# Kernel optimization log

Hardware: AMD Instinct MI355X
Metric: run time of the kernel (lower is better)

## Reference

```python
import jax, jax.numpy as jnp
import numpy as np

LR = 0.01        # memory update learning rate (init kwarg lr)
INIT_SCALE = 0.01
B, N, D = 8, 1024, 256


def setup_inputs() -> dict:
    key = jax.random.key(0)
    k1, k2, k3, k4, k5 = jax.random.split(key, 5)
    return {
        "sequence": jax.random.normal(k1, (B, N, D), dtype=jnp.float32),
        "targets": jax.random.normal(k2, (B, N, D), dtype=jnp.float32),
        "theta0": jax.random.normal(k3, (D, D), dtype=jnp.float32) * INIT_SCALE,
        "W_e": jax.random.normal(k4, (D, D), dtype=jnp.float32) * INIT_SCALE,
        "W_o": jax.random.normal(k5, (D, D), dtype=jnp.float32) * INIT_SCALE,
    }


def reference(sequence, targets, theta0, W_e, W_o):
    # process_sequence on (batch, n, d) with targets: theta is reset to theta0
    # for each batch element, then updated sequentially per token (delta rule).
    def step(theta, xt):
        x_t, tgt_t = xt                      # (d,), (d,)
        h = W_e @ x_t                        # encode: F.linear(x, W_e)
        pred = theta @ h                     # predict with current memory
        err = tgt_t - pred
        theta_new = theta + LR * jnp.outer(err, h)   # rank-1 fast-weight update
        out = W_o @ pred                     # output projection of PREDICTION
        return theta_new, out

    def per_batch(seq_b, tgt_b):             # (n, d), (n, d)
        _, outs = jax.lax.scan(step, theta0, (seq_b, tgt_b))
        return outs                          # (n, d)

    return jax.vmap(per_batch)(sequence, targets)   # (batch, n, d)
```

## Files before the change

### kernel.cpp

```cpp
#include <hip/hip_runtime.h>

#define LR_C 0.01f
#define NB 8
#define NTOK 1024
#define DD 256
#define CH 8
#define NCHUNK (NTOK / CH)

#define DPP_ADD(x, ctrl) \
    ((x) + __int_as_float(__builtin_amdgcn_update_dpp( \
        0, __float_as_int(x), (ctrl), 0xF, 0xF, true)))

#define REDUCE_ALL64(s) do { \
    s = DPP_ADD(s, 0xB1); \
    s = DPP_ADD(s, 0x4E); \
    s = DPP_ADD(s, 0x141); \
    s = DPP_ADD(s, 0x140); \
    s += __shfl_xor(s, 16, 64); \
    s += __shfl_xor(s, 32, 64); \
} while (0)

#define TBM 64
#define TBN 64
#define TBK 16

__global__ __launch_bounds__(256) void gemm_abt_kernel(
    const float* __restrict__ A, const float* __restrict__ B,
    float* __restrict__ C)
{
    __shared__ float As[TBK][TBM + 4];
    __shared__ float Bs[TBK][TBN + 4];
    const int t    = threadIdx.x;
    const int lrow = t >> 2, lk = (t & 3) * 4;
    const int tx   = t & 15, ty = t >> 4;

    const float* Ap = A + (size_t)(blockIdx.x * TBM + lrow) * DD + lk;
    const float* Bp = B + (size_t)(blockIdx.y * TBN + lrow) * DD + lk;

    float4 acc[4];
    #pragma unroll
    for (int i = 0; i < 4; ++i) acc[i] = make_float4(0.f, 0.f, 0.f, 0.f);

    float4 a0 = *reinterpret_cast<const float4*>(Ap);
    float4 b0 = *reinterpret_cast<const float4*>(Bp);

    for (int k0 = 0; k0 < DD; k0 += TBK) {
        __syncthreads();
        As[lk + 0][lrow] = a0.x; As[lk + 1][lrow] = a0.y;
        As[lk + 2][lrow] = a0.z; As[lk + 3][lrow] = a0.w;
        Bs[lk + 0][lrow] = b0.x; Bs[lk + 1][lrow] = b0.y;
        Bs[lk + 2][lrow] = b0.z; Bs[lk + 3][lrow] = b0.w;
        __syncthreads();
        if (k0 + TBK < DD) {
            a0 = *reinterpret_cast<const float4*>(Ap + k0 + TBK);
            b0 = *reinterpret_cast<const float4*>(Bp + k0 + TBK);
        }
        #pragma unroll
        for (int k = 0; k < TBK; ++k) {
            float4 av = *reinterpret_cast<const float4*>(&As[k][ty * 4]);
            float4 bv = *reinterpret_cast<const float4*>(&Bs[k][tx * 4]);
            acc[0].x = fmaf(av.x, bv.x, acc[0].x); acc[0].y = fmaf(av.x, bv.y, acc[0].y);
            acc[0].z = fmaf(av.x, bv.z, acc[0].z); acc[0].w = fmaf(av.x, bv.w, acc[0].w);
            acc[1].x = fmaf(av.y, bv.x, acc[1].x); acc[1].y = fmaf(av.y, bv.y, acc[1].y);
            acc[1].z = fmaf(av.y, bv.z, acc[1].z); acc[1].w = fmaf(av.y, bv.w, acc[1].w);
            acc[2].x = fmaf(av.z, bv.x, acc[2].x); acc[2].y = fmaf(av.z, bv.y, acc[2].y);
            acc[2].z = fmaf(av.z, bv.z, acc[2].z); acc[2].w = fmaf(av.z, bv.w, acc[2].w);
            acc[3].x = fmaf(av.w, bv.x, acc[3].x); acc[3].y = fmaf(av.w, bv.y, acc[3].y);
            acc[3].z = fmaf(av.w, bv.z, acc[3].z); acc[3].w = fmaf(av.w, bv.w, acc[3].w);
        }
    }
    #pragma unroll
    for (int i = 0; i < 4; ++i) {
        float* cp = C + (size_t)(blockIdx.x * TBM + ty * 4 + i) * DD
                      + blockIdx.y * TBN + tx * 4;
        *reinterpret_cast<float4*>(cp) = acc[i];
    }
}

__global__ __launch_bounds__(256) void gemm_pt_kernel(
    const float* __restrict__ PT, const float* __restrict__ B,
    float* __restrict__ C)
{
    __shared__ float As[TBK][TBM + 4];
    __shared__ float Bs[TBK][TBN + 4];
    const int t  = threadIdx.x;
    const int mb = blockIdx.x;
    const int b  = mb >> 4;
    const int t0 = (mb & 15) * TBM;
    const int bn = blockIdx.y;

    const int akrow = t >> 4, amcol = (t & 15) * 4;
    const int brow  = t >> 2, bk    = (t & 3) * 4;
    const int tx    = t & 15, ty    = t >> 4;

    const float* Ap = PT + (size_t)b * DD * NTOK + (size_t)akrow * NTOK + t0 + amcol;
    const float* Bp = B + (size_t)(bn * TBN + brow) * DD + bk;

    float4 acc[4];
    #pragma unroll
    for (int i = 0; i < 4; ++i) acc[i] = make_float4(0.f, 0.f, 0.f, 0.f);

    float4 a0 = *reinterpret_cast<const float4*>(Ap);
    float4 b0 = *reinterpret_cast<const float4*>(Bp);

    for (int k0 = 0; k0 < DD; k0 += TBK) {
        __syncthreads();
        *reinterpret_cast<float4*>(&As[akrow][amcol]) = a0;
        Bs[bk + 0][brow] = b0.x; Bs[bk + 1][brow] = b0.y;
        Bs[bk + 2][brow] = b0.z; Bs[bk + 3][brow] = b0.w;
        __syncthreads();
        if (k0 + TBK < DD) {
            a0 = *reinterpret_cast<const float4*>(Ap + (size_t)(k0 + TBK) * NTOK);
            b0 = *reinterpret_cast<const float4*>(Bp + k0 + TBK);
        }
        #pragma unroll
        for (int k = 0; k < TBK; ++k) {
            float4 av = *reinterpret_cast<const float4*>(&As[k][ty * 4]);
            float4 bv = *reinterpret_cast<const float4*>(&Bs[k][tx * 4]);
            acc[0].x = fmaf(av.x, bv.x, acc[0].x); acc[0].y = fmaf(av.x, bv.y, acc[0].y);
            acc[0].z = fmaf(av.x, bv.z, acc[0].z); acc[0].w = fmaf(av.x, bv.w, acc[0].w);
            acc[1].x = fmaf(av.y, bv.x, acc[1].x); acc[1].y = fmaf(av.y, bv.y, acc[1].y);
            acc[1].z = fmaf(av.y, bv.z, acc[1].z); acc[1].w = fmaf(av.y, bv.w, acc[1].w);
            acc[2].x = fmaf(av.z, bv.x, acc[2].x); acc[2].y = fmaf(av.z, bv.y, acc[2].y);
            acc[2].z = fmaf(av.z, bv.z, acc[2].z); acc[2].w = fmaf(av.z, bv.w, acc[2].w);
            acc[3].x = fmaf(av.w, bv.x, acc[3].x); acc[3].y = fmaf(av.w, bv.y, acc[3].y);
            acc[3].z = fmaf(av.w, bv.z, acc[3].z); acc[3].w = fmaf(av.w, bv.w, acc[3].w);
        }
    }
    #pragma unroll
    for (int i = 0; i < 4; ++i) {
        float* cp = C + (size_t)(b * NTOK + t0 + ty * 4 + i) * DD
                      + bn * TBN + tx * 4;
        *reinterpret_cast<float4*>(cp) = acc[i];
    }
}

__global__ __launch_bounds__(128) void gram_kernel(
    const float* __restrict__ H, float* __restrict__ Gram)
{
    const int blk  = blockIdx.x;
    const int b    = blk & 7;
    const int chk  = blk >> 3;
    const int w    = threadIdx.x >> 6;
    const int lane = threadIdx.x & 63;
    const float* Hc = H + ((size_t)b * NTOK + (size_t)chk * CH) * DD + lane * 4;

    float4 h[CH];
    #pragma unroll
    for (int i = 0; i < CH; ++i)
        h[i] = *reinterpret_cast<const float4*>(Hc + (size_t)i * DD);

    float sel = 0.f;
    #pragma unroll
    for (int i = 1; i < CH; ++i) {
        #pragma unroll
        for (int j = 0; j < i; ++j) {
            const int idx = i * (i - 1) / 2 + j;
            if ((idx & 1) == w) {
                float s = h[j].x * h[i].x;
                s = fmaf(h[j].y, h[i].y, s);
                s = fmaf(h[j].z, h[i].z, s);
                s = fmaf(h[j].w, h[i].w, s);
                REDUCE_ALL64(s);
                sel = (lane == idx) ? s : sel;
            }
        }
    }
    if (lane < 28 && (lane & 1) == w)
        Gram[((size_t)b * NCHUNK + chk) * 32 + lane] = sel;
}

#define GC(Cb, q) (((const float*)&(Cb)[0])[(q)])

#define STEP(HC, TC, CC, HN, TN, CN, ch) do { \
    const int nc_ = ((ch) + 1 < NCHUNK) ? (ch) + 1 : NCHUNK - 1; \
    const float* hsrc_ = Hb + (size_t)nc_ * CH * DD; \
    const float* tsrc_ = Tb + (size_t)nc_ * CH * DD; \
    const float4* gsrc_ = reinterpret_cast<const float4*>(Gb + nc_ * 32); \
    _Pragma("unroll") \
    for (int i_ = 0; i_ < CH; ++i_) { \
        HN[i_] = *reinterpret_cast<const float4*>(hsrc_ + (size_t)i_ * DD); \
        TN[i_] = LR_C * tsrc_[(size_t)i_ * DD]; \
    } \
    _Pragma("unroll") \
    for (int q_ = 0; q_ < 7; ++q_) CN[q_] = gsrc_[q_]; \
    __builtin_amdgcn_sched_barrier(0); \
    float a_[CH]; \
    _Pragma("unroll") \
    for (int i_ = 0; i_ < CH; ++i_) { \
        float s_ = HC[i_].x * th.x; \
        s_ = fmaf(HC[i_].y, th.y, s_); \
        s_ = fmaf(HC[i_].z, th.z, s_); \
        s_ = fmaf(HC[i_].w, th.w, s_); \
        REDUCE_ALL64(s_); \
        a_[i_] = s_; \
    } \
    float e_[CH], p_[CH]; \
    _Pragma("unroll") \
    for (int i_ = 0; i_ < CH; ++i_) { \
        float pv_ = a_[i_]; \
        _Pragma("unroll") \
        for (int j_ = 0; j_ < i_; ++j_) \
            pv_ = fmaf(e_[j_], GC(CC, i_ * (i_ - 1) / 2 + j_), pv_); \
        p_[i_] = pv_; \
        e_[i_] = fmaf(-LR_C, pv_, TC[i_]); \
    } \
    _Pragma("unroll") \
    for (int j_ = 0; j_ < CH; ++j_) { \
        th.x = fmaf(e_[j_], HC[j_].x, th.x); \
        th.y = fmaf(e_[j_], HC[j_].y, th.y); \
        th.z = fmaf(e_[j_], HC[j_].z, th.z); \
        th.w = fmaf(e_[j_], HC[j_].w, th.w); \
    } \
    float sel_ = p_[0]; \
    _Pragma("unroll") \
    for (int i_ = 1; i_ < CH; ++i_) sel_ = (lane == i_) ? p_[i_] : sel_; \
    if (lane < CH) Pb[(ch) * CH + lane] = sel_; \
} while (0)

__global__ __launch_bounds__(64, 2) void theta_scan_kernel(
    const float* __restrict__ H, const float* __restrict__ Tgt,
    const float* __restrict__ theta0, const float* __restrict__ Gram,
    float* __restrict__ PT)
{
    const int blk  = blockIdx.x;
    const int b    = blk & 7;
    const int row  = blk >> 3;
    const int lane = threadIdx.x;

    float4 th = *reinterpret_cast<const float4*>(
        theta0 + (size_t)row * DD + lane * 4);

    const float* Hb = H    + (size_t)b * NTOK * DD + lane * 4;
    const float* Tb = Tgt  + (size_t)b * NTOK * DD + row;
    const float* Gb = Gram + (size_t)b * NCHUNK * 32;
    float*       Pb = PT   + ((size_t)b * DD + row) * NTOK;

    float4 hA[CH]; float tA[CH]; float4 cA[7];
    float4 hB[CH]; float tB[CH]; float4 cB[7];

    #pragma unroll
    for (int i = 0; i < CH; ++i) {
        hA[i] = *reinterpret_cast<const float4*>(Hb + (size_t)i * DD);
        tA[i] = LR_C * Tb[(size_t)i * DD];
    }
    #pragma unroll
    for (int q = 0; q < 7; ++q)
        cA[q] = reinterpret_cast<const float4*>(Gb)[q];

    for (int ch = 0; ch < NCHUNK; ch += 2) {
        STEP(hA, tA, cA, hB, tB, cB, ch);
        STEP(hB, tB, cB, hA, tA, cA, ch + 1);
    }
}

extern "C" void kernel_launch(void* const* d_in, const int* in_sizes, int n_in,
                              void* d_out, int out_size, void* d_ws, size_t ws_size,
                              hipStream_t stream) {
    const float* seq    = (const float*)d_in[0];
    const float* tgt    = (const float*)d_in[1];
    const float* theta0 = (const float*)d_in[2];
    const float* W_e    = (const float*)d_in[3];
    const float* W_o    = (const float*)d_in[4];
    float* out = (float*)d_out;

    float* Hbuf  = (float*)d_ws;
    float* PTbuf = Hbuf + (size_t)NB * NTOK * DD;
    float* Cbuf = out;

    dim3 ggrid(NB * NTOK / TBM, DD / TBN);

    gemm_abt_kernel<<<ggrid, 256, 0, stream>>>(seq, W_e, Hbuf);
    gram_kernel<<<NB * NCHUNK, 128, 0, stream>>>(Hbuf, Cbuf);
    theta_scan_kernel<<<NB * 256, 64, 0, stream>>>(Hbuf, tgt, theta0, Cbuf, PTbuf);
    gemm_pt_kernel<<<ggrid, 256, 0, stream>>>(PTbuf, W_o, out);
}
```

Baseline: 213.9 us.

## Share H chunks across four theta rows via LDS async loads; enlarge GEMM tiles

The theta scan now runs four rows per 256-thread block. Each chunk of H, targets and Gram coefficients is loaded once into double-buffered LDS with global_load_lds, instead of each 64-lane block fetching it separately into registers. The eight per-token dot-product reductions are batched through an LDS transpose followed by a short DPP reduction and readlane, replacing eight full cross-lane reductions. Both GEMMs switch to 128x64 tiles with 512 threads. In exchange this adds block-wide barriers every chunk of the serial scan and relies on async LDS loads completing before those barriers.

New measurement: 216.3 us. About the same (+1.1%).

```diff
diff --git a/kernel.cpp b/kernel.cpp
--- a/kernel.cpp
+++ b/kernel.cpp
@@ -20,22 +20,34 @@
     s += __shfl_xor(s, 32, 64); \
 } while (0)
 
-#define TBM 64
-#define TBN 64
-#define TBK 16
-
-__global__ __launch_bounds__(256) void gemm_abt_kernel(
+__device__ __forceinline__ void gload16(const float* g, float* l) {
+    __builtin_amdgcn_global_load_lds(
+        (const __attribute__((address_space(1))) unsigned int*)g,
+        (__attribute__((address_space(3))) unsigned int*)l, 16, 0, 0);
+}
+__device__ __forceinline__ void gload4(const float* g, float* l) {
+    __builtin_amdgcn_global_load_lds(
+        (const __attribute__((address_space(1))) unsigned int*)g,
+        (__attribute__((address_space(3))) unsigned int*)l, 4, 0, 0);
+}
+
+#define GM 128
+#define GN 64
+#define GK 16
+
+__global__ __launch_bounds__(512) void gemm_abt_kernel(
     const float* __restrict__ A, const float* __restrict__ B,
     float* __restrict__ C)
 {
-    __shared__ float As[TBK][TBM + 4];
-    __shared__ float Bs[TBK][TBN + 4];
+    __shared__ float As[GK][GM + 4];
+    __shared__ float Bs[GK][GN + 4];
     const int t    = threadIdx.x;
-    const int lrow = t >> 2, lk = (t & 3) * 4;
+    const int arow = t >> 2, ak = (t & 3) * 4;
+    const int brow = t >> 2, bk = (t & 3) * 4;
     const int tx   = t & 15, ty = t >> 4;
 
-    const float* Ap = A + (size_t)(blockIdx.x * TBM + lrow) * DD + lk;
-    const float* Bp = B + (size_t)(blockIdx.y * TBN + lrow) * DD + lk;
+    const float* Ap = A + (size_t)(blockIdx.x * GM + arow) * DD + ak;
+    const float* Bp = B + (size_t)(blockIdx.y * GN + (t < 256 ? brow : 0)) * DD + bk;
 
     float4 acc[4];
     #pragma unroll
@@ -44,19 +56,21 @@
     float4 a0 = *reinterpret_cast<const float4*>(Ap);
     float4 b0 = *reinterpret_cast<const float4*>(Bp);
 
-    for (int k0 = 0; k0 < DD; k0 += TBK) {
-        __syncthreads();
-        As[lk + 0][lrow] = a0.x; As[lk + 1][lrow] = a0.y;
-        As[lk + 2][lrow] = a0.z; As[lk + 3][lrow] = a0.w;
-        Bs[lk + 0][lrow] = b0.x; Bs[lk + 1][lrow] = b0.y;
-        Bs[lk + 2][lrow] = b0.z; Bs[lk + 3][lrow] = b0.w;
-        __syncthreads();
-        if (k0 + TBK < DD) {
-            a0 = *reinterpret_cast<const float4*>(Ap + k0 + TBK);
-            b0 = *reinterpret_cast<const float4*>(Bp + k0 + TBK);
-        }
-        #pragma unroll
-        for (int k = 0; k < TBK; ++k) {
+    for (int k0 = 0; k0 < DD; k0 += GK) {
+        __syncthreads();
+        As[ak + 0][arow] = a0.x; As[ak + 1][arow] = a0.y;
+        As[ak + 2][arow] = a0.z; As[ak + 3][arow] = a0.w;
+        if (t < 256) {
+            Bs[bk + 0][brow] = b0.x; Bs[bk + 1][brow] = b0.y;
+            Bs[bk + 2][brow] = b0.z; Bs[bk + 3][brow] = b0.w;
+        }
+        __syncthreads();
+        if (k0 + GK < DD) {
+            a0 = *reinterpret_cast<const float4*>(Ap + k0 + GK);
+            b0 = *reinterpret_cast<const float4*>(Bp + k0 + GK);
+        }
+        #pragma unroll
+        for (int k = 0; k < GK; ++k) {
             float4 av = *reinterpret_cast<const float4*>(&As[k][ty * 4]);
             float4 bv = *reinterpret_cast<const float4*>(&Bs[k][tx * 4]);
             acc[0].x = fmaf(av.x, bv.x, acc[0].x); acc[0].y = fmaf(av.x, bv.y, acc[0].y);
@@ -71,30 +85,29 @@
     }
     #pragma unroll
     for (int i = 0; i < 4; ++i) {
-        float* cp = C + (size_t)(blockIdx.x * TBM + ty * 4 + i) * DD
-                      + blockIdx.y * TBN + tx * 4;
+        float* cp = C + (size_t)(blockIdx.x * GM + ty * 4 + i) * DD
+                      + blockIdx.y * GN + tx * 4;
         *reinterpret_cast<float4*>(cp) = acc[i];
     }
 }
 
-__global__ __launch_bounds__(256) void gemm_pt_kernel(
+__global__ __launch_bounds__(512) void gemm_pt_kernel(
     const float* __restrict__ PT, const float* __restrict__ B,
     float* __restrict__ C)
 {
-    __shared__ float As[TBK][TBM + 4];
-    __shared__ float Bs[TBK][TBN + 4];
+    __shared__ float As[GK][GM + 4];
+    __shared__ float Bs[GK][GN + 4];
     const int t  = threadIdx.x;
     const int mb = blockIdx.x;
-    const int b  = mb >> 4;
-    const int t0 = (mb & 15) * TBM;
-    const int bn = blockIdx.y;
-
-    const int akrow = t >> 4, amcol = (t & 15) * 4;
-    const int brow  = t >> 2, bk    = (t & 3) * 4;
-    const int tx    = t & 15, ty    = t >> 4;
-
-    const float* Ap = PT + (size_t)b * DD * NTOK + (size_t)akrow * NTOK + t0 + amcol;
-    const float* Bp = B + (size_t)(bn * TBN + brow) * DD + bk;
+    const int b  = mb >> 3;
+    const int t0 = (mb & 7) * GM;
+
+    const int krow = t >> 5, tcol = (t & 31) * 4;
+    const int brow = t >> 2, bk   = (t & 3) * 4;
+    const int tx   = t & 15, ty   = t >> 4;
+
+    const float* Ap = PT + (size_t)b * DD * NTOK + (size_t)krow * NTOK + t0 + tcol;
+    const float* Bp = B + (size_t)(blockIdx.y * GN + (t < 256 ? brow : 0)) * DD + bk;
 
     float4 acc[4];
     #pragma unroll
@@ -103,18 +116,20 @@
     float4 a0 = *reinterpret_cast<const float4*>(Ap);
     float4 b0 = *reinterpret_cast<const float4*>(Bp);
 
-    for (int k0 = 0; k0 < DD; k0 += TBK) {
-        __syncthreads();
-        *reinterpret_cast<float4*>(&As[akrow][amcol]) = a0;
-        Bs[bk + 0][brow] = b0.x; Bs[bk + 1][brow] = b0.y;
-        Bs[bk + 2][brow] = b0.z; Bs[bk + 3][brow] = b0.w;
-        __syncthreads();
-        if (k0 + TBK < DD) {
-            a0 = *reinterpret_cast<const float4*>(Ap + (size_t)(k0 + TBK) * NTOK);
-            b0 = *reinterpret_cast<const float4*>(Bp + k0 + TBK);
-        }
-        #pragma unroll
-        for (int k = 0; k < TBK; ++k) {
+    for (int k0 = 0; k0 < DD; k0 += GK) {
+        __syncthreads();
+        *reinterpret_cast<float4*>(&As[krow][tcol]) = a0;
+        if (t < 256) {
+            Bs[bk + 0][brow] = b0.x; Bs[bk + 1][brow] = b0.y;
+            Bs[bk + 2][brow] = b0.z; Bs[bk + 3][brow] = b0.w;
+        }
+        __syncthreads();
+        if (k0 + GK < DD) {
+            a0 = *reinterpret_cast<const float4*>(Ap + (size_t)(k0 + GK) * NTOK);
+            b0 = *reinterpret_cast<const float4*>(Bp + k0 + GK);
+        }
+        #pragma unroll
+        for (int k = 0; k < GK; ++k) {
             float4 av = *reinterpret_cast<const float4*>(&As[k][ty * 4]);
             float4 bv = *reinterpret_cast<const float4*>(&Bs[k][tx * 4]);
             acc[0].x = fmaf(av.x, bv.x, acc[0].x); acc[0].y = fmaf(av.x, bv.y, acc[0].y);
@@ -130,7 +145,7 @@
     #pragma unroll
     for (int i = 0; i < 4; ++i) {
         float* cp = C + (size_t)(b * NTOK + t0 + ty * 4 + i) * DD
-                      + bn * TBN + tx * 4;
+                      + blockIdx.y * GN + tx * 4;
         *reinterpret_cast<float4*>(cp) = acc[i];
     }
 }
@@ -170,87 +185,116 @@
         Gram[((size_t)b * NCHUNK + chk) * 32 + lane] = sel;
 }
 
-#define GC(Cb, q) (((const float*)&(Cb)[0])[(q)])
-
-#define STEP(HC, TC, CC, HN, TN, CN, ch) do { \
-    const int nc_ = ((ch) + 1 < NCHUNK) ? (ch) + 1 : NCHUNK - 1; \
-    const float* hsrc_ = Hb + (size_t)nc_ * CH * DD; \
-    const float* tsrc_ = Tb + (size_t)nc_ * CH * DD; \
-    const float4* gsrc_ = reinterpret_cast<const float4*>(Gb + nc_ * 32); \
-    _Pragma("unroll") \
-    for (int i_ = 0; i_ < CH; ++i_) { \
-        HN[i_] = *reinterpret_cast<const float4*>(hsrc_ + (size_t)i_ * DD); \
-        TN[i_] = LR_C * tsrc_[(size_t)i_ * DD]; \
-    } \
-    _Pragma("unroll") \
-    for (int q_ = 0; q_ < 7; ++q_) CN[q_] = gsrc_[q_]; \
-    __builtin_amdgcn_sched_barrier(0); \
-    float a_[CH]; \
-    _Pragma("unroll") \
-    for (int i_ = 0; i_ < CH; ++i_) { \
-        float s_ = HC[i_].x * th.x; \
-        s_ = fmaf(HC[i_].y, th.y, s_); \
-        s_ = fmaf(HC[i_].z, th.z, s_); \
-        s_ = fmaf(HC[i_].w, th.w, s_); \
-        REDUCE_ALL64(s_); \
-        a_[i_] = s_; \
-    } \
-    float e_[CH], p_[CH]; \
-    _Pragma("unroll") \
-    for (int i_ = 0; i_ < CH; ++i_) { \
-        float pv_ = a_[i_]; \
-        _Pragma("unroll") \
-        for (int j_ = 0; j_ < i_; ++j_) \
-            pv_ = fmaf(e_[j_], GC(CC, i_ * (i_ - 1) / 2 + j_), pv_); \
-        p_[i_] = pv_; \
-        e_[i_] = fmaf(-LR_C, pv_, TC[i_]); \
-    } \
-    _Pragma("unroll") \
-    for (int j_ = 0; j_ < CH; ++j_) { \
-        th.x = fmaf(e_[j_], HC[j_].x, th.x); \
-        th.y = fmaf(e_[j_], HC[j_].y, th.y); \
-        th.z = fmaf(e_[j_], HC[j_].z, th.z); \
-        th.w = fmaf(e_[j_], HC[j_].w, th.w); \
-    } \
-    float sel_ = p_[0]; \
-    _Pragma("unroll") \
-    for (int i_ = 1; i_ < CH; ++i_) sel_ = (lane == i_) ? p_[i_] : sel_; \
-    if (lane < CH) Pb[(ch) * CH + lane] = sel_; \
-} while (0)
-
-__global__ __launch_bounds__(64, 2) void theta_scan_kernel(
+__global__ __launch_bounds__(256, 2) void theta_scan_kernel(
     const float* __restrict__ H, const float* __restrict__ Tgt,
     const float* __restrict__ theta0, const float* __restrict__ Gram,
     float* __restrict__ PT)
 {
-    const int blk  = blockIdx.x;
-    const int b    = blk & 7;
-    const int row  = blk >> 3;
-    const int lane = threadIdx.x;
+    __shared__ float Hbuf[2][CH][DD];
+    __shared__ float Scr[4][CH][64];
+    __shared__ float TGb[2][64];
+    __shared__ float GRb[2][64];
+
+    const int b    = blockIdx.x & 7;
+    const int rb   = blockIdx.x >> 3;
+    const int wid  = threadIdx.x >> 6;
+    const int lane = threadIdx.x & 63;
+    const int row  = rb * 4 + wid;
 
     float4 th = *reinterpret_cast<const float4*>(
         theta0 + (size_t)row * DD + lane * 4);
 
-    const float* Hb = H    + (size_t)b * NTOK * DD + lane * 4;
-    const float* Tb = Tgt  + (size_t)b * NTOK * DD + row;
+    const float* Hb = H   + (size_t)b * NTOK * DD;
+    const float* Tb = Tgt + (size_t)b * NTOK * DD;
     const float* Gb = Gram + (size_t)b * NCHUNK * 32;
-    float*       Pb = PT   + ((size_t)b * DD + row) * NTOK;
-
-    float4 hA[CH]; float tA[CH]; float4 cA[7];
-    float4 hB[CH]; float tB[CH]; float4 cB[7];
-
-    #pragma unroll
-    for (int i = 0; i < CH; ++i) {
-        hA[i] = *reinterpret_cast<const float4*>(Hb + (size_t)i * DD);
-        tA[i] = LR_C * Tb[(size_t)i * DD];
-    }
-    #pragma unroll
-    for (int q = 0; q < 7; ++q)
-        cA[q] = reinterpret_cast<const float4*>(Gb)[q];
-
-    for (int ch = 0; ch < NCHUNK; ch += 2) {
-        STEP(hA, tA, cA, hB, tB, cB, ch);
-        STEP(hB, tB, cB, hA, tA, cA, ch + 1);
+    float*       Pb = PT  + ((size_t)b * DD + row) * NTOK;
+
+    const int ll = lane & 31;
+    const int tt = ll & 7, rr = ll >> 3;
+
+    {
+        const float* g0 = Hb + (size_t)(2 * wid) * DD + lane * 4;
+        gload16(g0,      &Hbuf[0][2 * wid][0]);
+        gload16(g0 + DD, &Hbuf[0][2 * wid + 1][0]);
+        if (wid == 0)
+            gload4(Tb + (size_t)tt * DD + rb * 4 + rr, &TGb[0][0]);
+        if (wid == 1)
+            gload4(Gb + ll, &GRb[0][0]);
+    }
+
+    for (int ch = 0; ch < NCHUNK; ++ch) {
+        const int par = ch & 1;
+        __syncthreads();
+
+        if (ch + 1 < NCHUNK) {
+            const int np = par ^ 1;
+            const float* g0 = Hb + (size_t)((ch + 1) * CH + 2 * wid) * DD + lane * 4;
+            gload16(g0,      &Hbuf[np][2 * wid][0]);
+            gload16(g0 + DD, &Hbuf[np][2 * wid + 1][0]);
+            if (wid == 0)
+                gload4(Tb + (size_t)((ch + 1) * CH + tt) * DD + rb * 4 + rr,
+                       &TGb[np][0]);
+            if (wid == 1)
+                gload4(Gb + (ch + 1) * 32 + ll, &GRb[np][0]);
+        }
+
+        float4 hh[CH]; float s[CH];
+        #pragma unroll
+        for (int i = 0; i < CH; ++i) {
+            hh[i] = *reinterpret_cast<const float4*>(&Hbuf[par][i][lane * 4]);
+            float sv = hh[i].x * th.x;
+            sv = fmaf(hh[i].y, th.y, sv);
+            sv = fmaf(hh[i].z, th.z, sv);
+            sv = fmaf(hh[i].w, th.w, sv);
+            s[i] = sv;
+        }
+        #pragma unroll
+        for (int i = 0; i < CH; ++i) Scr[wid][i][lane] = s[i];
+        const float* sb = &Scr[wid][0][0];
+        float4 r0 = *reinterpret_cast<const float4*>(sb + lane * 8);
+        float4 r1 = *reinterpret_cast<const float4*>(sb + lane * 8 + 4);
+        float sum = ((r0.x + r0.y) + (r0.z + r0.w))
+                  + ((r1.x + r1.y) + (r1.z + r1.w));
+        sum = DPP_ADD(sum, 0xB1);
+        sum = DPP_ADD(sum, 0x4E);
+        sum = DPP_ADD(sum, 0x141);
+        float a[CH];
+        #pragma unroll
+        for (int i = 0; i < CH; ++i)
+            a[i] = __int_as_float(
+                __builtin_amdgcn_readlane(__float_as_int(sum), 8 * i));
+
+        const float4* tb4 = reinterpret_cast<const float4*>(&TGb[par][wid * 8]);
+        float4 tg0 = tb4[0], tg1 = tb4[1];
+        float lt[CH] = {LR_C * tg0.x, LR_C * tg0.y, LR_C * tg0.z, LR_C * tg0.w,
+                        LR_C * tg1.x, LR_C * tg1.y, LR_C * tg1.z, LR_C * tg1.w};
+        const float4* gb4 = reinterpret_cast<const float4*>(&GRb[par][0]);
+        float gv[28];
+        #pragma unroll
+        for (int q = 0; q < 7; ++q)
+            *reinterpret_cast<float4*>(&gv[q * 4]) = gb4[q];
+
+        float e[CH], p[CH];
+        #pragma unroll
+        for (int i = 0; i < CH; ++i) {
+            float pv = a[i];
+            #pragma unroll
+            for (int j = 0; j < i; ++j)
+                pv = fmaf(e[j], gv[i * (i - 1) / 2 + j], pv);
+            p[i] = pv;
+            e[i] = fmaf(-LR_C, pv, lt[i]);
+        }
+        #pragma unroll
+        for (int j = 0; j < CH; ++j) {
+            th.x = fmaf(e[j], hh[j].x, th.x);
+            th.y = fmaf(e[j], hh[j].y, th.y);
+            th.z = fmaf(e[j], hh[j].z, th.z);
+            th.w = fmaf(e[j], hh[j].w, th.w);
+        }
+        float sel = p[0];
+        #pragma unroll
+        for (int i = 1; i < CH; ++i) sel = (lane == i) ? p[i] : sel;
+        if (lane < CH) Pb[ch * CH + lane] = sel;
     }
 }
 
@@ -266,12 +310,12 @@
 
     float* Hbuf  = (float*)d_ws;
     float* PTbuf = Hbuf + (size_t)NB * NTOK * DD;
-    float* Cbuf = out;
-
-    dim3 ggrid(NB * NTOK / TBM, DD / TBN);
-
-    gemm_abt_kernel<<<ggrid, 256, 0, stream>>>(seq, W_e, Hbuf);
+    float* Cbuf  = out;
+
+    dim3 ggrid(NB * NTOK / GM, DD / GN);
+
+    gemm_abt_kernel<<<ggrid, 512, 0, stream>>>(seq, W_e, Hbuf);
     gram_kernel<<<NB * NCHUNK, 128, 0, stream>>>(Hbuf, Cbuf);
-    theta_scan_kernel<<<NB * 256, 64, 0, stream>>>(Hbuf, tgt, theta0, Cbuf, PTbuf);
-    gemm_pt_kernel<<<ggrid, 256, 0, stream>>>(PTbuf, W_o, out);
-}
+    theta_scan_kernel<<<NB * 64, 256, 0, stream>>>(Hbuf, tgt, theta0, Cbuf, PTbuf);
+    gemm_pt_kernel<<<ggrid, 512, 0, stream>>>(PTbuf, W_o, out);
+}
```
